# Kernel optimization log

Hardware: AMD Instinct MI355X
Metric: run time of the kernel (lower is better)

Reference implementation:

```python
import jax, jax.numpy as jnp
import numpy as np

NU = 200000   # num user nodes
NI = 200000   # num item nodes
E = 500000    # edges per relation
D = 128       # in_feats
H = 128       # h_feats
NEG_SLOPE = 0.01  # F.leaky_relu default


def _sage(x_src, x_dst, src, dst, n_dst, W_self, W_neigh, b):
    # DGL SAGEConv('mean'): fc_self(x_dst) + fc_neigh(mean of in-neighbors) + bias
    msg = x_src[src]                                   # [E, d] gather
    agg = jax.ops.segment_sum(msg, dst, num_segments=n_dst)   # [n_dst, d]
    deg = jax.ops.segment_sum(jnp.ones((src.shape[0],), x_src.dtype), dst,
                              num_segments=n_dst)      # [n_dst]
    mean = agg / jnp.maximum(deg, 1.0)[:, None]        # zero in-degree -> 0
    return x_dst @ W_self + mean @ W_neigh + b


def setup_inputs() -> dict:
    key = jax.random.key(0)
    ks = jax.random.split(key, 20)
    s = 1.0 / np.sqrt(D)
    inp = {
        'x_user': jax.random.normal(ks[0], (NU, D), jnp.float32),
        'x_item': jax.random.normal(ks[1], (NI, D), jnp.float32),
        'w1_self_uc': jax.random.normal(ks[2], (D, H), jnp.float32) * s,
        'w1_neigh_uc': jax.random.normal(ks[3], (D, H), jnp.float32) * s,
        'b1_uc': jnp.zeros((H,), jnp.float32),
        'w1_self_iu': jax.random.normal(ks[4], (D, H), jnp.float32) * s,
        'w1_neigh_iu': jax.random.normal(ks[5], (D, H), jnp.float32) * s,
        'b1_iu': jnp.zeros((H,), jnp.float32),
        'w2_self_uc': jax.random.normal(ks[6], (H, H), jnp.float32) * s,
        'w2_neigh_uc': jax.random.normal(ks[7], (H, H), jnp.float32) * s,
        'b2_uc': jnp.zeros((H,), jnp.float32),
        'w2_self_iu': jax.random.normal(ks[8], (H, H), jnp.float32) * s,
        'w2_neigh_iu': jax.random.normal(ks[9], (H, H), jnp.float32) * s,
        'b2_iu': jnp.zeros((H,), jnp.float32),
        'src_uc': jax.random.randint(ks[10], (E,), 0, NU, jnp.int32),
        'dst_uc': jax.random.randint(ks[11], (E,), 0, NI, jnp.int32),
        'src_iu': jax.random.randint(ks[12], (E,), 0, NI, jnp.int32),
        'dst_iu': jax.random.randint(ks[13], (E,), 0, NU, jnp.int32),
    }
    return inp


def reference(x_user, x_item,
              w1_self_uc, w1_neigh_uc, b1_uc, w1_self_iu, w1_neigh_iu, b1_iu,
              w2_self_uc, w2_neigh_uc, b2_uc, w2_self_iu, w2_neigh_iu, b2_iu,
              src_uc, dst_uc, src_iu, dst_iu):
    # layer 1: relation 'clicks' user->item, relation 'clicked_by' item->user
    h1_item = _sage(x_user, x_item, src_uc, dst_uc, NI, w1_self_uc, w1_neigh_uc, b1_uc)
    h1_user = _sage(x_item, x_user, src_iu, dst_iu, NU, w1_self_iu, w1_neigh_iu, b1_iu)
    h1_item = jax.nn.leaky_relu(h1_item, NEG_SLOPE)
    h1_user = jax.nn.leaky_relu(h1_user, NEG_SLOPE)
    # layer 2
    h2_item = _sage(h1_user, h1_item, src_uc, dst_uc, NI, w2_self_uc, w2_neigh_uc, b2_uc)
    h2_user = _sage(h1_item, h1_user, src_iu, dst_iu, NU, w2_self_iu, w2_neigh_iu, b2_iu)
    # stack [user, item] (same shape) for a single output tensor
    return jnp.stack([h2_user, h2_item], axis=0)  # [2, 200000, 128]
```

## Files before the change

### kernel.cpp

```cpp
#include <hip/hip_runtime.h>
#include <hip/hip_bf16.h>

#define D_ 128

typedef __attribute__((ext_vector_type(8))) short s8b;
typedef __attribute__((ext_vector_type(4))) float f4;

union U4 { uint u[4]; s8b v; uint4 q; };

__device__ __forceinline__ void gl16(const void* g, void* lds) {
    __builtin_amdgcn_global_load_lds(
        (const __attribute__((address_space(1))) void*)g,
        (__attribute__((address_space(3))) void*)lds, 16, 0, 0);
}

__device__ __forceinline__ void split2(float f0, float f1, uint& hp, uint& lp) {
    uint u0 = __float_as_uint(f0), u1 = __float_as_uint(f1);
    hp = (u0 >> 16) | (u1 & 0xffff0000u);
    float r0 = f0 - __uint_as_float(u0 & 0xffff0000u);
    float r1 = f1 - __uint_as_float(u1 & 0xffff0000u);
    uint v0 = __float_as_uint(r0), v1 = __float_as_uint(r1);
    uint l0 = (v0 + 0x7fffu + ((v0 >> 16) & 1u)) >> 16;
    uint l1 = (v1 + 0x7fffu + ((v1 >> 16) & 1u)) >> 16;
    lp = l0 | (l1 << 16);
}

__global__ void deg2_kernel(const int* __restrict__ dstA, const int* __restrict__ dstB,
                            int* __restrict__ degA, int* __restrict__ degB, int E) {
    int e = blockIdx.x * blockDim.x + threadIdx.x;
    const int* dst = blockIdx.y ? dstB : dstA;
    int* deg = blockIdx.y ? degB : degA;
    if (e < E) atomicAdd(&deg[dst[e]], 1);
}

__global__ __launch_bounds__(256)
void scan1m(const int* __restrict__ degA, const int* __restrict__ degB,
            int* __restrict__ rpA, int* __restrict__ rpB,
            int* __restrict__ partA, int* __restrict__ partB, int N) {
    const int* deg = blockIdx.y ? degB : degA;
    int* rp = blockIdx.y ? rpB : rpA;
    int* partials = blockIdx.y ? partB : partA;
    int tid = threadIdx.x;
    int i = blockIdx.x * 256 + tid;
    int v = (i < N) ? deg[i] : 0;
    int lane = tid & 63, wid = tid >> 6;
    int x = v;
#pragma unroll
    for (int off = 1; off < 64; off <<= 1) {
        int y = __shfl_up(x, off, 64);
        if (lane >= off) x += y;
    }
    __shared__ int wsum[5];
    if (lane == 63) wsum[wid] = x;
    __syncthreads();
    if (tid == 0) {
        int a = wsum[0], b = wsum[1], c = wsum[2], d = wsum[3];
        wsum[0] = 0; wsum[1] = a; wsum[2] = a + b; wsum[3] = a + b + c;
        wsum[4] = a + b + c + d;
    }
    __syncthreads();
    if (i < N) rp[i] = wsum[wid] + x - v;
    if (tid == 0) partials[blockIdx.x] = wsum[4];
}

__global__ __launch_bounds__(1024)
void scan2m(int* __restrict__ partA, int* __restrict__ partB, int B) {
    int* partials = blockIdx.x ? partB : partA;
    __shared__ int buf[1024];
    int t = threadIdx.x;
    int v = (t < B) ? partials[t] : 0;
    buf[t] = v;
    __syncthreads();
    for (int off = 1; off < 1024; off <<= 1) {
        int add = (t >= off) ? buf[t - off] : 0;
        __syncthreads();
        buf[t] += add;
        __syncthreads();
    }
    if (t < B) partials[t] = buf[t] - v;
}

__global__ __launch_bounds__(256)
void scan3m(int* __restrict__ rpA, int* __restrict__ rpB,
            const int* __restrict__ partA, const int* __restrict__ partB, int N, int E) {
    int* rp = blockIdx.y ? rpB : rpA;
    const int* partials = blockIdx.y ? partB : partA;
    int i = blockIdx.x * 256 + threadIdx.x;
    if (i < N) rp[i] += partials[blockIdx.x];
    if (i == 0) rp[N] = E;
}

__global__ void fill2_csr(const int* __restrict__ srcA, const int* __restrict__ dstA,
                          const int* __restrict__ rpA, int* __restrict__ curA,
                          int* __restrict__ colA, int* __restrict__ colpA,
                          const int* __restrict__ srcB, const int* __restrict__ dstB,
                          const int* __restrict__ rpB, int* __restrict__ curB,
                          int* __restrict__ colB, int* __restrict__ colpB, int E) {
    int e = blockIdx.x * blockDim.x + threadIdx.x;
    if (e >= E) return;
    const int* src = blockIdx.y ? srcB : srcA;
    const int* dst = blockIdx.y ? dstB : dstA;
    const int* rp  = blockIdx.y ? rpB : rpA;
    int* cursor = blockIdx.y ? curB : curA;
    int* col    = blockIdx.y ? colB : colA;
    int* colp   = blockIdx.y ? colpB : colpA;
    int d = dst[e];
    int s = src[e];
    int idx = atomicAdd(&cursor[d], 1);
    col[rp[d] + idx] = s;
    if (idx < 4) colp[d * 4 + idx] = s;
}

__global__ __launch_bounds__(256)
void prep_weights(const float* __restrict__ s0, const float* __restrict__ n0,
                  const float* __restrict__ s1, const float* __restrict__ n1,
                  const float* __restrict__ s2, const float* __restrict__ n2,
                  const float* __restrict__ s3, const float* __restrict__ n3,
                  ushort* __restrict__ WTH, ushort* __restrict__ WTL) {
    int g = blockIdx.y;
    int t = blockIdx.x * 256 + threadIdx.x;
    int c = t & 127;
    int oct = t >> 7;
    const float* self  = g == 0 ? s0 : g == 1 ? s1 : g == 2 ? s2 : s3;
    const float* neigh = g == 0 ? n0 : g == 1 ? n1 : g == 2 ? n2 : n3;
    uint hd[4], ld_[4];
#pragma unroll
    for (int p = 0; p < 4; ++p) {
        uint hpair = 0, lpair = 0;
#pragma unroll
        for (int q = 0; q < 2; ++q) {
            int kv = oct * 8 + p * 2 + q;
            const float* Wsrc = kv < 128 ? self : neigh;
            float f = Wsrc[(size_t)(kv & 127) * 128 + c];
            uint u = __float_as_uint(f);
            uint h = u >> 16;
            float r = f - __uint_as_float(u & 0xffff0000u);
            uint v = __float_as_uint(r);
            uint l = (v + 0x7fffu + ((v >> 16) & 1u)) >> 16;
            hpair |= h << (16 * q);
            lpair |= l << (16 * q);
        }
        hd[p] = hpair; ld_[p] = lpair;
    }
    size_t base = ((size_t)g * 128 + c) * 256 + oct * 8;
    *(uint4*)(WTH + base) = make_uint4(hd[0], hd[1], hd[2], hd[3]);
    *(uint4*)(WTL + base) = make_uint4(ld_[0], ld_[1], ld_[2], ld_[3]);
}

#define AGGH 0
#define AGGL 16384
#define ASTEP 32768
#define WHO 40960
#define WLO 49152

template<int FP32IN, int SPLIT, int LRELU>
__device__ __forceinline__ void fused_body(const char* A1, const char* XN,
        const int* rp, const int* col, const int* colp,
        const ushort* WTh, const ushort* WTl, const float* bias, void* outp,
        int bid, char* smem) {
    const int t = threadIdx.x;
    const int row0 = bid * 64;

    {
        const int li = t & 15;
#pragma unroll
        for (int pass = 0; pass < 2; ++pass) {
            int nl = pass * 32 + (t >> 4);
            int node = row0 + nl;
            int beg = rp[node], end = rp[node + 1];
            int dg = end - beg;
            int4 c4 = *(const int4*)(colp + (size_t)node * 4);
            int s0 = dg > 0 ? c4.x : 0;
            int s1 = dg > 1 ? c4.y : 0;
            int s2 = dg > 2 ? c4.z : 0;
            int s3 = dg > 3 ? c4.w : 0;
            float w0 = dg > 0 ? 1.f : 0.f;
            float w1 = dg > 1 ? 1.f : 0.f;
            float w2 = dg > 2 ? 1.f : 0.f;
            float w3 = dg > 3 ? 1.f : 0.f;
            float a[8];
#pragma unroll
            for (int j = 0; j < 8; ++j) a[j] = 0.f;
            if (FP32IN) {
                const char* p0 = XN + (size_t)s0 * 512 + li * 32;
                const char* p1 = XN + (size_t)s1 * 512 + li * 32;
                const char* p2 = XN + (size_t)s2 * 512 + li * 32;
                const char* p3 = XN + (size_t)s3 * 512 + li * 32;
                float4 A0 = *(const float4*)p0, B0 = *(const float4*)(p0 + 16);
                float4 A1v = *(const float4*)p1, B1 = *(const float4*)(p1 + 16);
                float4 A2v = *(const float4*)p2, B2 = *(const float4*)(p2 + 16);
                float4 A3v = *(const float4*)p3, B3 = *(const float4*)(p3 + 16);
                float e0[8] = {A0.x, A0.y, A0.z, A0.w, B0.x, B0.y, B0.z, B0.w};
                float e1[8] = {A1v.x, A1v.y, A1v.z, A1v.w, B1.x, B1.y, B1.z, B1.w};
                float e2[8] = {A2v.x, A2v.y, A2v.z, A2v.w, B2.x, B2.y, B2.z, B2.w};
                float e3[8] = {A3v.x, A3v.y, A3v.z, A3v.w, B3.x, B3.y, B3.z, B3.w};
#pragma unroll
                for (int j = 0; j < 8; ++j)
                    a[j] = e0[j] * w0 + e1[j] * w1 + e2[j] * w2 + e3[j] * w3;
                for (int e = beg + 4; e < end; ++e) {
                    const char* p = XN + (size_t)col[e] * 512 + li * 32;
                    float4 X = *(const float4*)p, Y = *(const float4*)(p + 16);
                    a[0] += X.x; a[1] += X.y; a[2] += X.z; a[3] += X.w;
                    a[4] += Y.x; a[5] += Y.y; a[6] += Y.z; a[7] += Y.w;
                }
            } else {
                const char* p0 = XN + (size_t)s0 * 512 + li * 16;
                const char* p1 = XN + (size_t)s1 * 512 + li * 16;
                const char* p2 = XN + (size_t)s2 * 512 + li * 16;
                const char* p3 = XN + (size_t)s3 * 512 + li * 16;
                uint4 H0 = *(const uint4*)p0, L0 = *(const uint4*)(p0 + 256);
                uint4 H1 = *(const uint4*)p1, L1 = *(const uint4*)(p1 + 256);
                uint4 H2 = *(const uint4*)p2, L2 = *(const uint4*)(p2 + 256);
                uint4 H3 = *(const uint4*)p3, L3 = *(const uint4*)(p3 + 256);
                const ushort* hu; const ushort* lu;
#pragma unroll
                for (int q = 0; q < 4; ++q) {
                    uint4 H = q == 0 ? H0 : q == 1 ? H1 : q == 2 ? H2 : H3;
                    uint4 L = q == 0 ? L0 : q == 1 ? L1 : q == 2 ? L2 : L3;
                    float wq = q == 0 ? w0 : q == 1 ? w1 : q == 2 ? w2 : w3;
                    hu = (const ushort*)&H; lu = (const ushort*)&L;
#pragma unroll
                    for (int j = 0; j < 8; ++j) {
                        float v = __uint_as_float((uint)hu[j] << 16)
                                + __uint_as_float((uint)lu[j] << 16);
                        a[j] = fmaf(v, wq, a[j]);
                    }
                }
                for (int e = beg + 4; e < end; ++e) {
                    const char* p = XN + (size_t)col[e] * 512 + li * 16;
                    uint4 H = *(const uint4*)p, L = *(const uint4*)(p + 256);
                    hu = (const ushort*)&H; lu = (const ushort*)&L;
#pragma unroll
                    for (int j = 0; j < 8; ++j)
                        a[j] += __uint_as_float((uint)hu[j] << 16)
                              + __uint_as_float((uint)lu[j] << 16);
                }
            }
            float inv = 1.f / (float)(dg > 0 ? dg : 1);
            uint h[4], l[4];
            split2(a[0] * inv, a[1] * inv, h[0], l[0]);
            split2(a[2] * inv, a[3] * inv, h[1], l[1]);
            split2(a[4] * inv, a[5] * inv, h[2], l[2]);
            split2(a[6] * inv, a[7] * inv, h[3], l[3]);
            int chunk = li ^ (nl & 3) ^ (((nl >> 2) & 3) << 2);
            *(uint4*)(smem + AGGH + nl * 256 + chunk * 16) = make_uint4(h[0], h[1], h[2], h[3]);
            *(uint4*)(smem + AGGL + nl * 256 + chunk * 16) = make_uint4(l[0], l[1], l[2], l[3]);
        }
    }
    __syncthreads();

    const int w = t >> 6, lane = t & 63;
    const int fr = lane & 15, hi = lane >> 4;
    const int mrow0 = (w & 1) * 32, ncol0 = (w >> 1) * 32;

    f4 acc[2][2];
    {
        float bv[2];
#pragma unroll
        for (int n = 0; n < 2; ++n) bv[n] = bias[ncol0 + n * 16 + fr];
#pragma unroll
        for (int m = 0; m < 2; ++m)
#pragma unroll
            for (int n = 0; n < 2; ++n) acc[m][n] = (f4){bv[n], bv[n], bv[n], bv[n]};
    }

    for (int ks = 0; ks < 8; ++ks) {
        if (ks < 4) {
            if (FP32IN) {
                int row = t >> 3, cs = t & 7;
                gl16(A1 + (size_t)(row0 + row) * 512 + ks * 128 + ((cs ^ (row & 7)) * 16),
                     smem + ASTEP + t * 16);
            } else {
                int j = t & 255, part = t >> 8;
                int row = j >> 2, cs = j & 3;
                gl16(A1 + (size_t)(row0 + row) * 512 + part * 256 + ks * 64
                         + ((cs ^ ((row >> 1) & 3)) * 16),
                     smem + ASTEP + part * 4096 + j * 16);
            }
        }
        {
            int col_ = t >> 2, cs = t & 3;
            size_t so = (size_t)col_ * 512 + ks * 64 + ((cs ^ ((col_ >> 1) & 3)) * 16);
            gl16((const char*)WTh + so, smem + WHO + t * 16);
            gl16((const char*)WTl + so, smem + WLO + t * 16);
        }
        __syncthreads();

        s8b ah[2], al[2], wh[2], wl[2];
        if (ks < 4) {
            if (FP32IN) {
#pragma unroll
                for (int m = 0; m < 2; ++m) {
                    int r = mrow0 + m * 16 + fr;
                    f4 x0 = *(const f4*)(smem + ASTEP + r * 128 + (((hi * 2) ^ (r & 7)) * 16));
                    f4 x1 = *(const f4*)(smem + ASTEP + r * 128 + (((hi * 2 + 1) ^ (r & 7)) * 16));
                    U4 H, L;
                    split2(x0[0], x0[1], H.u[0], L.u[0]);
                    split2(x0[2], x0[3], H.u[1], L.u[1]);
                    split2(x1[0], x1[1], H.u[2], L.u[2]);
                    split2(x1[2], x1[3], H.u[3], L.u[3]);
                    ah[m] = H.v; al[m] = L.v;
                }
            } else {
#pragma unroll
                for (int m = 0; m < 2; ++m) {
                    int r = mrow0 + m * 16 + fr;
                    int off = r * 64 + ((hi ^ ((r >> 1) & 3)) * 16);
                    ah[m] = *(const s8b*)(smem + ASTEP + off);
                    al[m] = *(const s8b*)(smem + ASTEP + 4096 + off);
                }
            }
        } else {
            int kk = ks - 4;
#pragma unroll
            for (int m = 0; m < 2; ++m) {
                int r = mrow0 + m * 16 + fr;
                int chunk = (kk * 4 + hi) ^ (r & 3) ^ (((r >> 2) & 3) << 2);
                ah[m] = *(const s8b*)(smem + AGGH + r * 256 + chunk * 16);
                al[m] = *(const s8b*)(smem + AGGL + r * 256 + chunk * 16);
            }
        }
#pragma unroll
        for (int n = 0; n < 2; ++n) {
            int c = ncol0 + n * 16 + fr;
            int off = c * 64 + ((hi ^ ((c >> 1) & 3)) * 16);
            wh[n] = *(const s8b*)(smem + WHO + off);
            wl[n] = *(const s8b*)(smem + WLO + off);
        }
#pragma unroll
        for (int n = 0; n < 2; ++n)
#pragma unroll
            for (int m = 0; m < 2; ++m) {
                acc[m][n] = __builtin_amdgcn_mfma_f32_16x16x32_bf16(ah[m], wh[n], acc[m][n], 0, 0, 0);
                acc[m][n] = __builtin_amdgcn_mfma_f32_16x16x32_bf16(al[m], wh[n], acc[m][n], 0, 0, 0);
                acc[m][n] = __builtin_amdgcn_mfma_f32_16x16x32_bf16(ah[m], wl[n], acc[m][n], 0, 0, 0);
            }
        __syncthreads();
    }

    float* T = (float*)smem;
#pragma unroll
    for (int m = 0; m < 2; ++m)
#pragma unroll
        for (int n = 0; n < 2; ++n)
#pragma unroll
            for (int r = 0; r < 4; ++r)
                T[(mrow0 + m * 16 + hi * 4 + r) * 132 + ncol0 + n * 16 + fr] = acc[m][n][r];
    __syncthreads();
    {
        int row = t >> 3, q = t & 7;
        int gr = row0 + row;
        if (SPLIT) {
            char* ob = (char*)outp + (size_t)gr * 512;
#pragma unroll
            for (int i = 0; i < 2; ++i) {
                const float* p = T + row * 132 + (q * 2 + i) * 8;
                f4 x0 = *(const f4*)p;
                f4 x1 = *(const f4*)(p + 4);
                float e[8] = {x0[0], x0[1], x0[2], x0[3], x1[0], x1[1], x1[2], x1[3]};
                if (LRELU) {
#pragma unroll
                    for (int j = 0; j < 8; ++j) e[j] = e[j] > 0.f ? e[j] : 0.01f * e[j];
                }
                uint h[4], l[4];
#pragma unroll
                for (int j = 0; j < 4; ++j) split2(e[2 * j], e[2 * j + 1], h[j], l[j]);
                *(uint4*)(ob + (q * 2 + i) * 16) = make_uint4(h[0], h[1], h[2], h[3]);
                *(uint4*)(ob + 256 + (q * 2 + i) * 16) = make_uint4(l[0], l[1], l[2], l[3]);
            }
        } else {
            float* ob = (float*)outp + (size_t)gr * 128;
#pragma unroll
            for (int i = 0; i < 4; ++i) {
                f4 x = *(const f4*)(T + row * 132 + q * 16 + i * 4);
                float e0 = x[0], e1 = x[1], e2 = x[2], e3 = x[3];
                if (LRELU) {
                    e0 = e0 > 0.f ? e0 : 0.01f * e0;
                    e1 = e1 > 0.f ? e1 : 0.01f * e1;
                    e2 = e2 > 0.f ? e2 : 0.01f * e2;
                    e3 = e3 > 0.f ? e3 : 0.01f * e3;
                }
                *(float4*)(ob + q * 16 + i * 4) = make_float4(e0, e1, e2, e3);
            }
        }
    }
}

template<int FP32IN, int SPLIT, int LRELU>
__global__ __launch_bounds__(512, 2)
void fused2k(const void* A1a, const void* XNa, const int* rpA, const int* colA,
             const int* colpA, const ushort* WTha, const ushort* WTla,
             const float* ba, void* outa,
             const void* A1b, const void* XNb, const int* rpB, const int* colB,
             const int* colpB, const ushort* WThb, const ushort* WTlb,
             const float* bb, void* outb, int blocksA) {
    __shared__ __align__(16) char smem[57344];
    bool isA = (int)blockIdx.x < blocksA;
    int bid = isA ? blockIdx.x : blockIdx.x - blocksA;
    if (isA)
        fused_body<FP32IN, SPLIT, LRELU>((const char*)A1a, (const char*)XNa, rpA, colA,
                                         colpA, WTha, WTla, ba, outa, bid, smem);
    else
        fused_body<FP32IN, SPLIT, LRELU>((const char*)A1b, (const char*)XNb, rpB, colB,
                                         colpB, WThb, WTlb, bb, outb, bid, smem);
}

extern "C" void kernel_launch(void* const* d_in, const int* in_sizes, int n_in,
                              void* d_out, int out_size, void* d_ws, size_t ws_size,
                              hipStream_t stream) {
    const float* x_user     = (const float*)d_in[0];
    const float* x_item     = (const float*)d_in[1];
    const float* w1_self_uc = (const float*)d_in[2];
    const float* w1_neigh_uc= (const float*)d_in[3];
    const float* b1_uc      = (const float*)d_in[4];
    const float* w1_self_iu = (const float*)d_in[5];
    const float* w1_neigh_iu= (const float*)d_in[6];
    const float* b1_iu      = (const float*)d_in[7];
    const float* w2_self_uc = (const float*)d_in[8];
    const float* w2_neigh_uc= (const float*)d_in[9];
    const float* b2_uc      = (const float*)d_in[10];
    const float* w2_self_iu = (const float*)d_in[11];
    const float* w2_neigh_iu= (const float*)d_in[12];
    const float* b2_iu      = (const float*)d_in[13];
    const int* src_uc = (const int*)d_in[14];
    const int* dst_uc = (const int*)d_in[15];
    const int* src_iu = (const int*)d_in[16];
    const int* dst_iu = (const int*)d_in[17];

    const int NU = in_sizes[0] / D_;
    const int NI = in_sizes[1] / D_;
    const int E  = in_sizes[14];

    float* f_user = (float*)d_out;
    float* f_item = (float*)d_out + (size_t)NU * 128;

    char* ws = (char*)d_ws;
    const size_t FEAT_BYTES = (size_t)200000 * 512;
    char* h1_item  = ws;          ws += FEAT_BYTES;
    char* h1_user  = ws;          ws += FEAT_BYTES;
    ushort* WTH    = (ushort*)ws; ws += (size_t)4 * 128 * 256 * sizeof(ushort);
    ushort* WTL    = (ushort*)ws; ws += (size_t)4 * 128 * 256 * sizeof(ushort);
    int* colp_uc   = (int*)ws;    ws += (size_t)200000 * 4 * sizeof(int);
    int* colp_iu   = (int*)ws;    ws += (size_t)200000 * 4 * sizeof(int);
    int* rp_uc     = (int*)ws;    ws += (size_t)(NI + 1) * sizeof(int);
    int* rp_iu     = (int*)ws;    ws += (size_t)(NU + 1) * sizeof(int);
    int* col_uc    = (int*)ws;    ws += (size_t)E * sizeof(int);
    int* col_iu    = (int*)ws;    ws += (size_t)E * sizeof(int);
    int* deg_uc    = (int*)ws;    ws += (size_t)200000 * sizeof(int);
    int* deg_iu    = (int*)ws;    ws += (size_t)200000 * sizeof(int);
    int* cur_uc    = (int*)ws;    ws += (size_t)200000 * sizeof(int);
    int* cur_iu    = (int*)ws;    ws += (size_t)200000 * sizeof(int);
    int* partA     = (int*)ws;    ws += (size_t)1024 * sizeof(int);
    int* partB     = (int*)ws;    ws += (size_t)1024 * sizeof(int);

    const int TPB = 256;
    const int eBlocks  = (E + TPB - 1) / TPB;
    const int sBlocks  = (200000 + 255) / 256;
    const int mBlocksI = (NI + 63) / 64;
    const int mBlocksU = (NU + 63) / 64;
    const size_t WSTRIDE = (size_t)128 * 256;

    hipMemsetAsync(deg_uc, 0, (size_t)4 * 200000 * sizeof(int), stream);

    prep_weights<<<dim3(16, 4), 256, 0, stream>>>(
        w1_self_uc, w1_neigh_uc, w1_self_iu, w1_neigh_iu,
        w2_self_uc, w2_neigh_uc, w2_self_iu, w2_neigh_iu, WTH, WTL);

    deg2_kernel<<<dim3(eBlocks, 2), TPB, 0, stream>>>(dst_uc, dst_iu, deg_uc, deg_iu, E);
    scan1m<<<dim3(sBlocks, 2), 256, 0, stream>>>(deg_uc, deg_iu, rp_uc, rp_iu, partA, partB, 200000);
    scan2m<<<2, 1024, 0, stream>>>(partA, partB, sBlocks);
    scan3m<<<dim3(sBlocks, 2), 256, 0, stream>>>(rp_uc, rp_iu, partA, partB, 200000, E);
    fill2_csr<<<dim3(eBlocks, 2), TPB, 0, stream>>>(src_uc, dst_uc, rp_uc, cur_uc, col_uc, colp_uc,
                                                    src_iu, dst_iu, rp_iu, cur_iu, col_iu, colp_iu, E);

    fused2k<1, 1, 1><<<mBlocksI + mBlocksU, 512, 0, stream>>>(
        x_item, x_user, rp_uc, col_uc, colp_uc, WTH + 0 * WSTRIDE, WTL + 0 * WSTRIDE,
        b1_uc, h1_item,
        x_user, x_item, rp_iu, col_iu, colp_iu, WTH + 1 * WSTRIDE, WTL + 1 * WSTRIDE,
        b1_iu, h1_user, mBlocksI);

    fused2k<0, 0, 0><<<mBlocksI + mBlocksU, 512, 0, stream>>>(
        h1_item, h1_user, rp_uc, col_uc, colp_uc, WTH + 2 * WSTRIDE, WTL + 2 * WSTRIDE,
        b2_uc, f_item,
        h1_user, h1_item, rp_iu, col_iu, colp_iu, WTH + 3 * WSTRIDE, WTL + 3 * WSTRIDE,
        b2_iu, f_user, mBlocksI);
}
```

Measured before the change: 588.4 us.

## Prefetch first neighbor rows into registers and overlap with first GEMM stage

The fused kernel now issues the loads for each node's first four neighbor rows into registers at kernel start, before staging the first self-feature and weight tile. The mean aggregation into LDS then runs after that first stage is resident, and the first MFMA step follows, so gather latency can overlap the tile load. The launch bound is also raised from 2 to 4 blocks per CU, which tightens the register budget. That matters because the prefetched rows hold 64 extra VGPRs, so register spilling is a real risk, and the LDS size per block likely prevents 4 blocks from being resident anyway.

Measured after the change: 582.9 us. About the same (-0.9%).

```diff
diff --git a/kernel.cpp b/kernel.cpp
--- a/kernel.cpp
+++ b/kernel.cpp
@@ -23,6 +23,11 @@
     uint l0 = (v0 + 0x7fffu + ((v0 >> 16) & 1u)) >> 16;
     uint l1 = (v1 + 0x7fffu + ((v1 >> 16) & 1u)) >> 16;
     lp = l0 | (l1 << 16);
+}
+
+__device__ __forceinline__ float4 asf4(uint4 u) {
+    return make_float4(__uint_as_float(u.x), __uint_as_float(u.y),
+                       __uint_as_float(u.z), __uint_as_float(u.w));
 }
 
 __global__ void deg2_kernel(const int* __restrict__ dstA, const int* __restrict__ dstB,
@@ -160,111 +165,40 @@
         int bid, char* smem) {
     const int t = threadIdx.x;
     const int row0 = bid * 64;
-
-    {
-        const int li = t & 15;
-#pragma unroll
-        for (int pass = 0; pass < 2; ++pass) {
-            int nl = pass * 32 + (t >> 4);
-            int node = row0 + nl;
-            int beg = rp[node], end = rp[node + 1];
-            int dg = end - beg;
-            int4 c4 = *(const int4*)(colp + (size_t)node * 4);
-            int s0 = dg > 0 ? c4.x : 0;
-            int s1 = dg > 1 ? c4.y : 0;
-            int s2 = dg > 2 ? c4.z : 0;
-            int s3 = dg > 3 ? c4.w : 0;
-            float w0 = dg > 0 ? 1.f : 0.f;
-            float w1 = dg > 1 ? 1.f : 0.f;
-            float w2 = dg > 2 ? 1.f : 0.f;
-            float w3 = dg > 3 ? 1.f : 0.f;
-            float a[8];
-#pragma unroll
-            for (int j = 0; j < 8; ++j) a[j] = 0.f;
-            if (FP32IN) {
-                const char* p0 = XN + (size_t)s0 * 512 + li * 32;
-                const char* p1 = XN + (size_t)s1 * 512 + li * 32;
-                const char* p2 = XN + (size_t)s2 * 512 + li * 32;
-                const char* p3 = XN + (size_t)s3 * 512 + li * 32;
-                float4 A0 = *(const float4*)p0, B0 = *(const float4*)(p0 + 16);
-                float4 A1v = *(const float4*)p1, B1 = *(const float4*)(p1 + 16);
-                float4 A2v = *(const float4*)p2, B2 = *(const float4*)(p2 + 16);
-                float4 A3v = *(const float4*)p3, B3 = *(const float4*)(p3 + 16);
-                float e0[8] = {A0.x, A0.y, A0.z, A0.w, B0.x, B0.y, B0.z, B0.w};
-                float e1[8] = {A1v.x, A1v.y, A1v.z, A1v.w, B1.x, B1.y, B1.z, B1.w};
-                float e2[8] = {A2v.x, A2v.y, A2v.z, A2v.w, B2.x, B2.y, B2.z, B2.w};
-                float e3[8] = {A3v.x, A3v.y, A3v.z, A3v.w, B3.x, B3.y, B3.z, B3.w};
-#pragma unroll
-                for (int j = 0; j < 8; ++j)
-                    a[j] = e0[j] * w0 + e1[j] * w1 + e2[j] * w2 + e3[j] * w3;
-                for (int e = beg + 4; e < end; ++e) {
-                    const char* p = XN + (size_t)col[e] * 512 + li * 32;
-                    float4 X = *(const float4*)p, Y = *(const float4*)(p + 16);
-                    a[0] += X.x; a[1] += X.y; a[2] += X.z; a[3] += X.w;
-                    a[4] += Y.x; a[5] += Y.y; a[6] += Y.z; a[7] += Y.w;
-                }
-            } else {
-                const char* p0 = XN + (size_t)s0 * 512 + li * 16;
-                const char* p1 = XN + (size_t)s1 * 512 + li * 16;
-                const char* p2 = XN + (size_t)s2 * 512 + li * 16;
-                const char* p3 = XN + (size_t)s3 * 512 + li * 16;
-                uint4 H0 = *(const uint4*)p0, L0 = *(const uint4*)(p0 + 256);
-                uint4 H1 = *(const uint4*)p1, L1 = *(const uint4*)(p1 + 256);
-                uint4 H2 = *(const uint4*)p2, L2 = *(const uint4*)(p2 + 256);
-                uint4 H3 = *(const uint4*)p3, L3 = *(const uint4*)(p3 + 256);
-                const ushort* hu; const ushort* lu;
-#pragma unroll
-                for (int q = 0; q < 4; ++q) {
-                    uint4 H = q == 0 ? H0 : q == 1 ? H1 : q == 2 ? H2 : H3;
-                    uint4 L = q == 0 ? L0 : q == 1 ? L1 : q == 2 ? L2 : L3;
-                    float wq = q == 0 ? w0 : q == 1 ? w1 : q == 2 ? w2 : w3;
-                    hu = (const ushort*)&H; lu = (const ushort*)&L;
-#pragma unroll
-                    for (int j = 0; j < 8; ++j) {
-                        float v = __uint_as_float((uint)hu[j] << 16)
-                                + __uint_as_float((uint)lu[j] << 16);
-                        a[j] = fmaf(v, wq, a[j]);
-                    }
-                }
-                for (int e = beg + 4; e < end; ++e) {
-                    const char* p = XN + (size_t)col[e] * 512 + li * 16;
-                    uint4 H = *(const uint4*)p, L = *(const uint4*)(p + 256);
-                    hu = (const ushort*)&H; lu = (const ushort*)&L;
-#pragma unroll
-                    for (int j = 0; j < 8; ++j)
-                        a[j] += __uint_as_float((uint)hu[j] << 16)
-                              + __uint_as_float((uint)lu[j] << 16);
-                }
-            }
-            float inv = 1.f / (float)(dg > 0 ? dg : 1);
-            uint h[4], l[4];
-            split2(a[0] * inv, a[1] * inv, h[0], l[0]);
-            split2(a[2] * inv, a[3] * inv, h[1], l[1]);
-            split2(a[4] * inv, a[5] * inv, h[2], l[2]);
-            split2(a[6] * inv, a[7] * inv, h[3], l[3]);
-            int chunk = li ^ (nl & 3) ^ (((nl >> 2) & 3) << 2);
-            *(uint4*)(smem + AGGH + nl * 256 + chunk * 16) = make_uint4(h[0], h[1], h[2], h[3]);
-            *(uint4*)(smem + AGGL + nl * 256 + chunk * 16) = make_uint4(l[0], l[1], l[2], l[3]);
-        }
-    }
-    __syncthreads();
-
-    const int w = t >> 6, lane = t & 63;
-    const int fr = lane & 15, hi = lane >> 4;
-    const int mrow0 = (w & 1) * 32, ncol0 = (w >> 1) * 32;
-
-    f4 acc[2][2];
-    {
-        float bv[2];
-#pragma unroll
-        for (int n = 0; n < 2; ++n) bv[n] = bias[ncol0 + n * 16 + fr];
-#pragma unroll
-        for (int m = 0; m < 2; ++m)
-#pragma unroll
-            for (int n = 0; n < 2; ++n) acc[m][n] = (f4){bv[n], bv[n], bv[n], bv[n]};
-    }
-
-    for (int ks = 0; ks < 8; ++ks) {
+    const int li = t & 15;
+
+    uint4 GH[2][4], GL[2][4];
+    float wv[2][4];
+    int begv[2], endv[2], dgv[2];
+#pragma unroll
+    for (int p = 0; p < 2; ++p) {
+        int nl = p * 32 + (t >> 4);
+        int node = row0 + nl;
+        int beg = rp[node], end = rp[node + 1];
+        int dg = end - beg;
+        begv[p] = beg; endv[p] = end; dgv[p] = dg;
+        int4 c4 = *(const int4*)(colp + (size_t)node * 4);
+        int s0 = dg > 0 ? c4.x : 0;
+        int s1 = dg > 1 ? c4.y : 0;
+        int s2 = dg > 2 ? c4.z : 0;
+        int s3 = dg > 3 ? c4.w : 0;
+        wv[p][0] = dg > 0 ? 1.f : 0.f;
+        wv[p][1] = dg > 1 ? 1.f : 0.f;
+        wv[p][2] = dg > 2 ? 1.f : 0.f;
+        wv[p][3] = dg > 3 ? 1.f : 0.f;
+        const int lo = FP32IN ? li * 32 : li * 16;
+        const int d2 = FP32IN ? 16 : 256;
+        const char* p0 = XN + (size_t)s0 * 512 + lo;
+        const char* p1 = XN + (size_t)s1 * 512 + lo;
+        const char* p2 = XN + (size_t)s2 * 512 + lo;
+        const char* p3 = XN + (size_t)s3 * 512 + lo;
+        GH[p][0] = *(const uint4*)p0; GL[p][0] = *(const uint4*)(p0 + d2);
+        GH[p][1] = *(const uint4*)p1; GL[p][1] = *(const uint4*)(p1 + d2);
+        GH[p][2] = *(const uint4*)p2; GL[p][2] = *(const uint4*)(p2 + d2);
+        GH[p][3] = *(const uint4*)p3; GL[p][3] = *(const uint4*)(p3 + d2);
+    }
+
+    auto stage = [&](int ks) {
         if (ks < 4) {
             if (FP32IN) {
                 int row = t >> 3, cs = t & 7;
@@ -284,8 +218,24 @@
             gl16((const char*)WTh + so, smem + WHO + t * 16);
             gl16((const char*)WTl + so, smem + WLO + t * 16);
         }
-        __syncthreads();
-
+    };
+
+    const int w = t >> 6, lane = t & 63;
+    const int fr = lane & 15, hi = lane >> 4;
+    const int mrow0 = (w & 1) * 32, ncol0 = (w >> 1) * 32;
+
+    f4 acc[2][2];
+    {
+        float bv[2];
+#pragma unroll
+        for (int n = 0; n < 2; ++n) bv[n] = bias[ncol0 + n * 16 + fr];
+#pragma unroll
+        for (int m = 0; m < 2; ++m)
+#pragma unroll
+            for (int n = 0; n < 2; ++n) acc[m][n] = (f4){bv[n], bv[n], bv[n], bv[n]};
+    }
+
+    auto compute = [&](int ks) {
         s8b ah[2], al[2], wh[2], wl[2];
         if (ks < 4) {
             if (FP32IN) {
@@ -335,6 +285,75 @@
                 acc[m][n] = __builtin_amdgcn_mfma_f32_16x16x32_bf16(al[m], wh[n], acc[m][n], 0, 0, 0);
                 acc[m][n] = __builtin_amdgcn_mfma_f32_16x16x32_bf16(ah[m], wl[n], acc[m][n], 0, 0, 0);
             }
+    };
+
+    stage(0);
+    __syncthreads();
+
+#pragma unroll
+    for (int p = 0; p < 2; ++p) {
+        int nl = p * 32 + (t >> 4);
+        float a[8];
+#pragma unroll
+        for (int j = 0; j < 8; ++j) a[j] = 0.f;
+        if (FP32IN) {
+#pragma unroll
+            for (int q = 0; q < 4; ++q) {
+                float4 X = asf4(GH[p][q]);
+                float4 Y = asf4(GL[p][q]);
+                float wq = wv[p][q];
+                a[0] = fmaf(X.x, wq, a[0]); a[1] = fmaf(X.y, wq, a[1]);
+                a[2] = fmaf(X.z, wq, a[2]); a[3] = fmaf(X.w, wq, a[3]);
+                a[4] = fmaf(Y.x, wq, a[4]); a[5] = fmaf(Y.y, wq, a[5]);
+                a[6] = fmaf(Y.z, wq, a[6]); a[7] = fmaf(Y.w, wq, a[7]);
+            }
+            for (int e = begv[p] + 4; e < endv[p]; ++e) {
+                const char* pp = XN + (size_t)col[e] * 512 + li * 32;
+                float4 X = *(const float4*)pp, Y = *(const float4*)(pp + 16);
+                a[0] += X.x; a[1] += X.y; a[2] += X.z; a[3] += X.w;
+                a[4] += Y.x; a[5] += Y.y; a[6] += Y.z; a[7] += Y.w;
+            }
+        } else {
+#pragma unroll
+            for (int q = 0; q < 4; ++q) {
+                float wq = wv[p][q];
+                const ushort* hu = (const ushort*)&GH[p][q];
+                const ushort* lu = (const ushort*)&GL[p][q];
+#pragma unroll
+                for (int j = 0; j < 8; ++j) {
+                    float v = __uint_as_float((uint)hu[j] << 16)
+                            + __uint_as_float((uint)lu[j] << 16);
+                    a[j] = fmaf(v, wq, a[j]);
+                }
+            }
+            for (int e = begv[p] + 4; e < endv[p]; ++e) {
+                const char* pp = XN + (size_t)col[e] * 512 + li * 16;
+                uint4 H = *(const uint4*)pp, L = *(const uint4*)(pp + 256);
+                const ushort* hu = (const ushort*)&H;
+                const ushort* lu = (const ushort*)&L;
+#pragma unroll
+                for (int j = 0; j < 8; ++j)
+                    a[j] += __uint_as_float((uint)hu[j] << 16)
+                          + __uint_as_float((uint)lu[j] << 16);
+            }
+        }
+        float inv = 1.f / (float)(dgv[p] > 0 ? dgv[p] : 1);
+        uint h[4], l[4];
+        split2(a[0] * inv, a[1] * inv, h[0], l[0]);
+        split2(a[2] * inv, a[3] * inv, h[1], l[1]);
+        split2(a[4] * inv, a[5] * inv, h[2], l[2]);
+        split2(a[6] * inv, a[7] * inv, h[3], l[3]);
+        int chunk = li ^ (nl & 3) ^ (((nl >> 2) & 3) << 2);
+        *(uint4*)(smem + AGGH + nl * 256 + chunk * 16) = make_uint4(h[0], h[1], h[2], h[3]);
+        *(uint4*)(smem + AGGL + nl * 256 + chunk * 16) = make_uint4(l[0], l[1], l[2], l[3]);
+    }
+
+    compute(0);
+    __syncthreads();
+    for (int ks = 1; ks < 8; ++ks) {
+        stage(ks);
+        __syncthreads();
+        compute(ks);
         __syncthreads();
     }
 
@@ -387,7 +406,7 @@
 }
 
 template<int FP32IN, int SPLIT, int LRELU>
-__global__ __launch_bounds__(512, 2)
+__global__ __launch_bounds__(512, 4)
 void fused2k(const void* A1a, const void* XNa, const int* rpA, const int* colA,
              const int* colpA, const ushort* WTha, const ushort* WTla,
              const float* ba, void* outa,
```
